# Performance work log

Measured on AMD Instinct MI355X. Metric: run time of the kernel, lower is better.

Reference implementation:

```python
import jax, jax.numpy as jnp
import numpy as np

EPS = 1e-5

def _bn_relu(x, gamma, beta):
    # BatchNorm2d in training mode: biased batch stats over (B, H, W)
    mu = jnp.mean(x, axis=(0, 2, 3), keepdims=True)
    var = jnp.mean((x - mu) ** 2, axis=(0, 2, 3), keepdims=True)
    xh = (x - mu) * jax.lax.rsqrt(var + EPS)
    return jax.nn.relu(xh * gamma[None, :, None, None] + beta[None, :, None, None])

def setup_inputs() -> dict:
    key = jax.random.key(0)
    ks = jax.random.split(key, 16)
    B, N, D = 4, 256, 256            # in_channels = 2*D = 512
    feats = jax.random.normal(ks[0], (B, 1 + 2 * N, D), dtype=jnp.float32)
    def lin(k, o, c):
        return jax.random.normal(k, (o, c), dtype=jnp.float32) * (1.0 / np.sqrt(c))
    return {
        "feats": feats,
        "W1": lin(ks[1], 256, 512), "b1": jnp.zeros((256,), jnp.float32),
        "g1": jnp.ones((256,), jnp.float32), "be1": jnp.zeros((256,), jnp.float32),
        "W2": lin(ks[2], 128, 256), "b2": jnp.zeros((128,), jnp.float32),
        "g2": jnp.ones((128,), jnp.float32), "be2": jnp.zeros((128,), jnp.float32),
        "W3": lin(ks[3], 64, 128), "b3": jnp.zeros((64,), jnp.float32),
        "g3": jnp.ones((64,), jnp.float32), "be3": jnp.zeros((64,), jnp.float32),
        "W4": lin(ks[4], 1, 64), "b4": jnp.zeros((1,), jnp.float32),
    }

def reference(feats, W1, b1, g1, be1, W2, b2, g2, be2, W3, b3, g3, be3, W4, b4):
    B, T, Dfull = feats.shape
    f = feats[:, 1:]                                  # [B, 2N, D]
    N = f.shape[1] // 2
    D = f.shape[2]
    f = f.reshape(B, N, 2, D).mean(axis=2)            # [B, N, D]
    fc = jnp.transpose(f, (0, 2, 1))                  # [B, D, N]
    # conv1(cat(x, t)) fused: first D input channels see f_i, last D see f_j
    a = jnp.einsum('oc,bcn->bon', W1[:, :D], fc)      # [B, 256, N]
    bpart = jnp.einsum('oc,bcn->bon', W1[:, D:], fc)  # [B, 256, N]
    h = a[:, :, :, None] + bpart[:, :, None, :] + b1[None, :, None, None]  # [B,256,N,N]
    h = _bn_relu(h, g1, be1)
    h = jnp.einsum('oc,bcij->boij', W2, h) + b2[None, :, None, None]
    h = _bn_relu(h, g2, be2)
    h = jnp.einsum('oc,bcij->boij', W3, h) + b3[None, :, None, None]
    h = _bn_relu(h, g3, be3)
    h = jnp.einsum('oc,bcij->boij', W4, h) + b4[None, :, None, None]
    return h[:, 0]                                    # [B, N, N]
```

## Files before the change

### kernel.cpp

```cpp
#include <hip/hip_runtime.h>
#include <hip/hip_bf16.h>

#define EPS 1e-5f

typedef __attribute__((ext_vector_type(8))) short bf16x8;
typedef __attribute__((ext_vector_type(4))) float f32x4;

static constexpr size_t OFF_FT    = 0;
static constexpr size_t OFF_W1T   = 1048576;
static constexpr size_t OFF_W2B   = 1572864;
static constexpr size_t OFF_W3B   = 1638400;
static constexpr size_t OFF_S1    = 1654784;
static constexpr size_t OFF_T1    = 1655808;
static constexpr size_t OFF_ST2   = 1660928;
static constexpr size_t OFF_ABT   = 1703936;
static constexpr size_t OFF_H2T   = 4194304;
static constexpr size_t OFF_P1    = OFF_H2T;
static constexpr size_t OFF_H3T   = 71303168;

static __device__ inline float bfu2f(unsigned int u16) {
    return __uint_as_float(u16 << 16);
}
static __device__ inline unsigned short f2bfu(float f) {
    unsigned int u = __float_as_uint(f);
    unsigned int r = u + 0x7fffu + ((u >> 16) & 1u);
    return (unsigned short)(r >> 16);
}
static __device__ inline unsigned int pkbf(float lo, float hi) {
    __hip_bfloat162 p = __float22bfloat162_rn(make_float2(lo, hi));
    return *reinterpret_cast<unsigned int*>(&p);
}

static __device__ __forceinline__ uint2 bnpk4(float4 fv, const float* aa, const float* ss, int c) {
    float4 a4 = *(const float4*)(aa + c);
    float4 s4 = *(const float4*)(ss + c);
    float r0 = fmaxf(fmaf(fv.x, s4.x, a4.x), 0.f);
    float r1 = fmaxf(fmaf(fv.y, s4.y, a4.y), 0.f);
    float r2 = fmaxf(fmaf(fv.z, s4.z, a4.z), 0.f);
    float r3 = fmaxf(fmaf(fv.w, s4.w, a4.w), 0.f);
    return make_uint2(pkbf(r0, r1), pkbf(r2, r3));
}
static __device__ __forceinline__ uint2 bn2pk4(uint2 v, const float* ss, const float* tt, int c) {
    float4 s4 = *(const float4*)(ss + c);
    float4 t4 = *(const float4*)(tt + c);
    float r0 = fmaxf(fmaf(bfu2f(v.x & 0xffffu), s4.x, t4.x), 0.f);
    float r1 = fmaxf(fmaf(bfu2f(v.x >> 16),     s4.y, t4.y), 0.f);
    float r2 = fmaxf(fmaf(bfu2f(v.y & 0xffffu), s4.z, t4.z), 0.f);
    float r3 = fmaxf(fmaf(bfu2f(v.y >> 16),     s4.w, t4.w), 0.f);
    return make_uint2(pkbf(r0, r1), pkbf(r2, r3));
}

__global__ __launch_bounds__(256) void k0kt(const float* __restrict__ feats,
                                            const float* __restrict__ W1,
                                            const float* __restrict__ W2,
                                            const float* __restrict__ W3,
                                            float* __restrict__ fT, float* __restrict__ W1T,
                                            unsigned short* __restrict__ W2b,
                                            unsigned short* __restrict__ W3b,
                                            float* __restrict__ statsZero) {
    int bx = blockIdx.x, tid = threadIdx.x;
    if (bx < 128) {
        __shared__ float s[32][65];
        int b = bx >> 5, nt = (bx >> 2) & 7, ct = bx & 3;
        int n0 = nt * 32, c0 = ct * 64;
        const float* fb = feats + (size_t)b * 513 * 256;
        #pragma unroll
        for (int k = 0; k < 8; ++k) {
            int idx = tid + k * 256;
            int n = idx >> 6, c = idx & 63;
            const float* r = fb + (size_t)(1 + 2 * (n0 + n)) * 256 + c0 + c;
            s[n][c] = 0.5f * (r[0] + r[256]);
        }
        __syncthreads();
        #pragma unroll
        for (int k = 0; k < 8; ++k) {
            int idx = tid + k * 256;
            int c = idx >> 5, n = idx & 31;
            fT[((size_t)(b * 256) + c0 + c) * 256 + n0 + n] = s[n][c];
        }
    } else {
        if (bx == 128) {
            #pragma unroll
            for (int z = 0; z < 13; ++z) {
                int f = tid + z * 256;
                if (f < 3073) statsZero[f] = 0.f;
            }
        }
        int idx = (bx - 128) * 256 + tid;
        if (idx < 131072) {
            int c = idx >> 9, o = idx & 511;
            W1T[idx] = (o < 256) ? W1[(size_t)o * 512 + c] : W1[(size_t)(o - 256) * 512 + 256 + c];
        } else if (idx < 163840) {
            int j = idx - 131072;
            W2b[j] = f2bfu(W2[j]);
        } else if (idx < 172032) {
            int j = idx - 163840;
            W3b[j] = f2bfu(W3[j]);
        }
    }
}

__global__ __launch_bounds__(256) void k1_gemm(const float* __restrict__ W1T,
                                               const float* __restrict__ fT,
                                               float* __restrict__ abT,
                                               float2* __restrict__ part,
                                               const float* __restrict__ g1,
                                               const float* __restrict__ be1,
                                               float* __restrict__ s1,
                                               float* __restrict__ t1,
                                               unsigned int* __restrict__ counter) {
    __shared__ float sW[64][36];
    __shared__ float sF[64][68];
    int tid = threadIdx.x;
    int bx = blockIdx.x;
    int b = bx >> 2, n0 = (bx & 3) * 64;
    int o0 = blockIdx.y * 32;
    int og = tid >> 4, jq = tid & 15;
    float acc[2][4] = {};
    for (int c0 = 0; c0 < 256; c0 += 64) {
        #pragma unroll
        for (int k = 0; k < 8; ++k) {
            int idx = tid + k * 256;
            int c = idx >> 5, o = idx & 31;
            sW[c][o] = W1T[(size_t)(c0 + c) * 512 + o0 + o];
        }
        #pragma unroll
        for (int k = 0; k < 16; ++k) {
            int idx = tid + k * 256;
            int c = idx >> 6, n = idx & 63;
            sF[c][n] = fT[((size_t)(b * 256) + c0 + c) * 256 + n0 + n];
        }
        __syncthreads();
        #pragma unroll 8
        for (int c = 0; c < 64; ++c) {
            float4 rv = *(const float4*)&sF[c][jq * 4];
            float2 wv = *(const float2*)&sW[c][og * 2];
            float rr[4] = {rv.x, rv.y, rv.z, rv.w};
            #pragma unroll
            for (int w = 0; w < 4; ++w) {
                acc[0][w] = fmaf(wv.x, rr[w], acc[0][w]);
                acc[1][w] = fmaf(wv.y, rr[w], acc[1][w]);
            }
        }
        __syncthreads();
    }
    #pragma unroll
    for (int w = 0; w < 4; ++w) {
        int n = n0 + jq * 4 + w;
        *(float2*)&abT[((size_t)(b * 256) + n) * 512 + o0 + og * 2] =
            make_float2(acc[0][w], acc[1][w]);
    }
    #pragma unroll
    for (int m = 0; m < 2; ++m) {
        float s = 0.f, q = 0.f;
        #pragma unroll
        for (int w = 0; w < 4; ++w) { float v = acc[m][w]; s += v; q += v * v; }
        #pragma unroll
        for (int off = 8; off; off >>= 1) { s += __shfl_down(s, off); q += __shfl_down(q, off); }
        if (jq == 0) part[(size_t)bx * 512 + o0 + og * 2 + m] = make_float2(s, q);
    }
    __threadfence();
    __shared__ unsigned int lastFlag;
    if (tid == 0) lastFlag = (atomicAdd(counter, 1u) == 255u) ? 1u : 0u;
    __syncthreads();
    if (lastFlag) {
        int o = tid;
        float msum = 0.f, e2sum = 0.f;
        #pragma unroll
        for (int bb = 0; bb < 4; ++bb) {
            float Sa = 0.f, Qa = 0.f, Sb = 0.f, Qb = 0.f;
            #pragma unroll
            for (int nt = 0; nt < 4; ++nt) {
                float2 pa = part[(size_t)(bb * 4 + nt) * 512 + o];
                float2 pb = part[(size_t)(bb * 4 + nt) * 512 + 256 + o];
                Sa += pa.x; Qa += pa.y; Sb += pb.x; Qb += pb.y;
            }
            float ma = Sa * (1.f / 256.f), mb = Sb * (1.f / 256.f);
            msum += ma + mb;
            e2sum += Qa * (1.f / 256.f) + Qb * (1.f / 256.f) + 2.f * ma * mb;
        }
        float m = msum * 0.25f, e2 = e2sum * 0.25f;
        float var = e2 - m * m;
        float s = g1[o] * rsqrtf(var + EPS);
        s1[o] = s;
        t1[o] = be1[o] - m * s;
    }
}

__global__ __launch_bounds__(256) void k2_mfma(const float* __restrict__ abT,
                                               const unsigned short* __restrict__ W2b,
                                               const float* __restrict__ s1,
                                               const float* __restrict__ t1,
                                               unsigned short* __restrict__ h2T,
                                               float* __restrict__ gS2,
                                               float* __restrict__ gQ2) {
    __shared__ __align__(16) char smem[35840];
    float* aaS = (float*)smem;
    float* ssS = (float*)(smem + 1024);
    unsigned short* sW = (unsigned short*)(smem + 2048);
    unsigned short* sB = (unsigned short*)(smem + 12288);
    unsigned short* sT = (unsigned short*)smem;
    float* sS = (float*)(smem + 34816);
    float* sQ = (float*)(smem + 35328);

    int tid = threadIdx.x;
    int j0 = blockIdx.x * 128, i = blockIdx.y, b = blockIdx.z;

    {
        float av = abT[((size_t)(b * 256 + i)) * 512 + tid];
        float s = s1[tid];
        aaS[tid] = fmaf(av, s, t1[tid]);
        ssS[tid] = s;
    }
    if (tid < 128) { sS[tid] = 0.f; sQ[tid] = 0.f; }
    __syncthreads();

    int lane = tid & 63, wv = tid >> 6;
    int wr = wv >> 1, wc = wv & 1;
    int lo = lane & 15, khi = lane >> 4;
    int jrow = tid >> 1, half = tid & 1;

    const float* bpRow = abT + ((size_t)(b * 256 + j0 + jrow)) * 512 + 256 + half * 16;
    const unsigned short* wRow = W2b + jrow * 256 + half * 16;

    f32x4 acc[4][4] = {};

    for (int c0 = 0; c0 < 256; c0 += 32) {
        {
            uint4 v0 = *(const uint4*)(wRow + c0);
            uint4 v1 = *(const uint4*)(wRow + c0 + 8);
            uint4* dst = (uint4*)(sW + jrow * 40 + half * 16);
            dst[0] = v0; dst[1] = v1;
        }
        {
            float4 f0 = *(const float4*)(bpRow + c0);
            float4 f1 = *(const float4*)(bpRow + c0 + 4);
            float4 f2 = *(const float4*)(bpRow + c0 + 8);
            float4 f3 = *(const float4*)(bpRow + c0 + 12);
            int cb = c0 + half * 16;
            uint2 p0 = bnpk4(f0, aaS, ssS, cb);
            uint2 p1 = bnpk4(f1, aaS, ssS, cb + 4);
            uint2 p2 = bnpk4(f2, aaS, ssS, cb + 8);
            uint2 p3 = bnpk4(f3, aaS, ssS, cb + 12);
            uint4* dst = (uint4*)(sB + jrow * 40 + half * 16);
            dst[0] = make_uint4(p0.x, p0.y, p1.x, p1.y);
            dst[1] = make_uint4(p2.x, p2.y, p3.x, p3.y);
        }
        __syncthreads();
        const unsigned short* aB = sW + (wr * 64 + lo) * 40 + khi * 8;
        const unsigned short* bB = sB + (wc * 64 + lo) * 40 + khi * 8;
        bf16x8 af[4], bfr[4];
        #pragma unroll
        for (int fm = 0; fm < 4; ++fm) af[fm] = *(const bf16x8*)(aB + fm * 16 * 40);
        #pragma unroll
        for (int fn = 0; fn < 4; ++fn) bfr[fn] = *(const bf16x8*)(bB + fn * 16 * 40);
        #pragma unroll
        for (int fm = 0; fm < 4; ++fm)
            #pragma unroll
            for (int fn = 0; fn < 4; ++fn)
                acc[fm][fn] = __builtin_amdgcn_mfma_f32_16x16x32_bf16(af[fm], bfr[fn], acc[fm][fn], 0, 0, 0);
        __syncthreads();
    }

    #pragma unroll
    for (int fm = 0; fm < 4; ++fm)
        #pragma unroll
        for (int fn = 0; fn < 4; ++fn) {
            int oq = wr * 64 + fm * 16 + khi * 4;
            int j  = wc * 64 + fn * 16 + lo;
            *(uint2*)(sT + j * 136 + oq) =
                make_uint2(pkbf(acc[fm][fn][0], acc[fm][fn][1]),
                           pkbf(acc[fm][fn][2], acc[fm][fn][3]));
        }
    __syncthreads();
    {
        size_t gbase = (((size_t)(b * 256 + i)) * 256 + j0 + jrow) * 128 + half * 64;
        #pragma unroll
        for (int e = 0; e < 8; ++e) {
            uint4 v = *(const uint4*)(sT + jrow * 136 + half * 64 + e * 8);
            *(uint4*)(h2T + gbase + e * 8) = v;
        }
    }
    {
        int o = tid & 127, p = tid >> 7;
        const unsigned short* col = sT + (p * 64) * 136 + o;
        float s = 0.f, q = 0.f;
        for (int j = 0; j < 64; ++j) {
            float v = bfu2f(col[j * 136]);
            s += v; q += v * v;
        }
        atomicAdd(&sS[o], s);
        atomicAdd(&sQ[o], q);
    }
    __syncthreads();
    if (tid < 128) {
        int slot = (i & 7) * 128;
        atomicAdd(&gS2[slot + tid], sS[tid]);
        atomicAdd(&gQ2[slot + tid], sQ[tid]);
    }
}

__global__ __launch_bounds__(256) void k3_mfma(const unsigned short* __restrict__ h2T,
                                               const unsigned short* __restrict__ W3b,
                                               const float* __restrict__ gS2,
                                               const float* __restrict__ gQ2,
                                               const float* __restrict__ g2,
                                               const float* __restrict__ be2,
                                               unsigned short* __restrict__ h3T,
                                               float* __restrict__ gS3,
                                               float* __restrict__ gQ3) {
    __shared__ __align__(16) char smem[39424];
    float* s2S = (float*)smem;
    float* t2S = (float*)(smem + 512);
    unsigned short* sW3 = (unsigned short*)(smem + 1024);
    unsigned short* sB  = (unsigned short*)(smem + 18432);
    float* sS = (float*)(smem + 38912);
    float* sQ = (float*)(smem + 39168);
    unsigned short* sT  = (unsigned short*)(smem + 1024);

    int tid = threadIdx.x;
    int i = blockIdx.x, b = blockIdx.y;
    if (tid < 128) {
        float su = 0.f, qu = 0.f;
        #pragma unroll
        for (int k = 0; k < 8; ++k) { su += gS2[k * 128 + tid]; qu += gQ2[k * 128 + tid]; }
        float mean = su * (1.f / 262144.f);
        float var = qu * (1.f / 262144.f) - mean * mean;
        float sc = g2[tid] * rsqrtf(var + EPS);
        s2S[tid] = sc;
        t2S[tid] = be2[tid] - mean * sc;
    }
    if (tid < 64) { sS[tid] = 0.f; sQ[tid] = 0.f; }
    {
        int o = tid >> 2, qd = tid & 3;
        #pragma unroll
        for (int e = 0; e < 4; ++e) {
            uint4 v = *(const uint4*)(W3b + o * 128 + qd * 32 + e * 8);
            *(uint4*)(sW3 + o * 136 + qd * 32 + e * 8) = v;
        }
    }
    __syncthreads();

    int lane = tid & 63, wv = tid >> 6;
    int lo = lane & 15, khi = lane >> 4;

    f32x4 acc[4][4] = {};
    const unsigned short* src = h2T + (((size_t)(b * 256 + i)) * 256 + tid) * 128;

    for (int c0 = 0; c0 < 128; c0 += 32) {
        #pragma unroll
        for (int e = 0; e < 4; ++e) {
            uint4 v = *(const uint4*)(src + c0 + e * 8);
            int c = c0 + e * 8;
            uint2 pa = bn2pk4(make_uint2(v.x, v.y), s2S, t2S, c);
            uint2 pb = bn2pk4(make_uint2(v.z, v.w), s2S, t2S, c + 4);
            *(uint4*)(sB + tid * 40 + e * 8) = make_uint4(pa.x, pa.y, pb.x, pb.y);
        }
        __syncthreads();
        bf16x8 af[4], bfr[4];
        #pragma unroll
        for (int fm = 0; fm < 4; ++fm)
            af[fm] = *(const bf16x8*)(sW3 + (fm * 16 + lo) * 136 + c0 + khi * 8);
        #pragma unroll
        for (int fn = 0; fn < 4; ++fn)
            bfr[fn] = *(const bf16x8*)(sB + (wv * 64 + fn * 16 + lo) * 40 + khi * 8);
        #pragma unroll
        for (int fm = 0; fm < 4; ++fm)
            #pragma unroll
            for (int fn = 0; fn < 4; ++fn)
                acc[fm][fn] = __builtin_amdgcn_mfma_f32_16x16x32_bf16(af[fm], bfr[fn], acc[fm][fn], 0, 0, 0);
        __syncthreads();
    }

    #pragma unroll
    for (int fm = 0; fm < 4; ++fm)
        #pragma unroll
        for (int fn = 0; fn < 4; ++fn) {
            int oq = fm * 16 + khi * 4;
            int j  = wv * 64 + fn * 16 + lo;
            *(uint2*)(sT + j * 72 + oq) =
                make_uint2(pkbf(acc[fm][fn][0], acc[fm][fn][1]),
                           pkbf(acc[fm][fn][2], acc[fm][fn][3]));
        }
    __syncthreads();
    {
        size_t gbase = (((size_t)(b * 256 + i)) * 256 + tid) * 64;
        #pragma unroll
        for (int e = 0; e < 8; ++e) {
            uint4 v = *(const uint4*)(sT + tid * 72 + e * 8);
            *(uint4*)(h3T + gbase + e * 8) = v;
        }
    }
    {
        int o = tid & 63, p = tid >> 6;
        const unsigned short* col = sT + (p * 64) * 72 + o;
        float s = 0.f, q = 0.f;
        for (int j = 0; j < 64; ++j) {
            float v = bfu2f(col[j * 72]);
            s += v; q += v * v;
        }
        atomicAdd(&sS[o], s);
        atomicAdd(&sQ[o], q);
    }
    __syncthreads();
    if (tid < 64) {
        int slot = (i & 7) * 64;
        atomicAdd(&gS3[slot + tid], sS[tid]);
        atomicAdd(&gQ3[slot + tid], sQ[tid]);
    }
}

__global__ __launch_bounds__(256) void k4_final(const unsigned short* __restrict__ h3T,
                                                const float* __restrict__ W4,
                                                const float* __restrict__ gS3,
                                                const float* __restrict__ gQ3,
                                                const float* __restrict__ g3,
                                                const float* __restrict__ be3,
                                                const float* __restrict__ b4,
                                                float* __restrict__ out) {
    __shared__ __align__(16) char smem[37632];
    float* wS = (float*)smem;
    float* sS = (float*)(smem + 256);
    float* tS = (float*)(smem + 512);
    unsigned short* sL = (unsigned short*)(smem + 768);
    int tid = threadIdx.x;
    int i = blockIdx.x, b = blockIdx.y;
    if (tid < 64) {
        float su = 0.f, qu = 0.f;
        #pragma unroll
        for (int k = 0; k < 8; ++k) { su += gS3[k * 64 + tid]; qu += gQ3[k * 64 + tid]; }
        float mean = su * (1.f / 262144.f);
        float var = qu * (1.f / 262144.f) - mean * mean;
        float sc = g3[tid] * rsqrtf(var + EPS);
        wS[tid] = W4[tid];
        sS[tid] = sc;
        tS[tid] = be3[tid] - mean * sc;
    }
    const unsigned short* src = h3T + ((size_t)(b * 256 + i)) * 256 * 64;
    #pragma unroll
    for (int e = 0; e < 8; ++e) {
        int f = tid + 256 * e;
        uint4 v = *(const uint4*)(src + f * 8);
        *(uint4*)(sL + (f >> 3) * 72 + (f & 7) * 8) = v;
    }
    __syncthreads();
    float acc = 0.f;
    #pragma unroll
    for (int e = 0; e < 8; ++e) {
        uint4 v = *(const uint4*)(sL + tid * 72 + e * 8);
        unsigned int w[4] = {v.x, v.y, v.z, v.w};
        #pragma unroll
        for (int k = 0; k < 4; ++k) {
            int c = e * 8 + 2 * k;
            float f0 = bfu2f(w[k] & 0xffffu);
            float f1 = bfu2f(w[k] >> 16);
            acc += wS[c] * fmaxf(fmaf(f0, sS[c], tS[c]), 0.f);
            acc += wS[c + 1] * fmaxf(fmaf(f1, sS[c + 1], tS[c + 1]), 0.f);
        }
    }
    out[((size_t)(b * 256 + i)) * 256 + tid] = acc + b4[0];
}

extern "C" void kernel_launch(void* const* d_in, const int* in_sizes, int n_in,
                              void* d_out, int out_size, void* d_ws, size_t ws_size,
                              hipStream_t stream) {
    const float* feats = (const float*)d_in[0];
    const float* W1  = (const float*)d_in[1];
    const float* g1  = (const float*)d_in[3];
    const float* be1 = (const float*)d_in[4];
    const float* W2  = (const float*)d_in[5];
    const float* g2  = (const float*)d_in[7];
    const float* be2 = (const float*)d_in[8];
    const float* W3  = (const float*)d_in[9];
    const float* g3  = (const float*)d_in[11];
    const float* be3 = (const float*)d_in[12];
    const float* W4  = (const float*)d_in[13];
    const float* b4  = (const float*)d_in[14];

    char* ws = (char*)d_ws;
    float* fT   = (float*)(ws + OFF_FT);
    float* W1T  = (float*)(ws + OFF_W1T);
    unsigned short* W2b = (unsigned short*)(ws + OFF_W2B);
    unsigned short* W3b = (unsigned short*)(ws + OFF_W3B);
    float* abT  = (float*)(ws + OFF_ABT);
    float* s1   = (float*)(ws + OFF_S1);
    float* t1   = (float*)(ws + OFF_T1);
    float* gS2  = (float*)(ws + OFF_ST2);
    float* gQ2  = (float*)(ws + OFF_ST2 + 4096);
    float* gS3  = (float*)(ws + OFF_ST2 + 8192);
    float* gQ3  = (float*)(ws + OFF_ST2 + 10240);
    unsigned int* counter = (unsigned int*)(ws + OFF_ST2 + 12288);
    float2* part = (float2*)(ws + OFF_P1);
    unsigned short* h2T = (unsigned short*)(ws + OFF_H2T);
    unsigned short* h3T = (unsigned short*)(ws + OFF_H3T);
    float* out = (float*)d_out;

    k0kt<<<800, 256, 0, stream>>>(feats, W1, W2, W3, fT, W1T, W2b, W3b, (float*)(ws + OFF_ST2));
    k1_gemm<<<dim3(16, 16), 256, 0, stream>>>(W1T, fT, abT, part, g1, be1, s1, t1, counter);
    k2_mfma<<<dim3(2, 256, 4), 256, 0, stream>>>(abT, W2b, s1, t1, h2T, gS2, gQ2);
    k3_mfma<<<dim3(256, 4), 256, 0, stream>>>(h2T, W3b, gS2, gQ2, g2, be2, h3T, gS3, gQ3);
    k4_final<<<dim3(256, 4), 256, 0, stream>>>(h3T, W4, gS3, gQ3, g3, be3, b4, out);
}
```

Before: 220.5 us.

## Widen k2 tile to cover all 256 j columns per block

The second-layer MFMA kernel now has each block compute the full 256-wide j range for one (i,b) row instead of two 128-wide halves. The point is to load each W2 tile into shared memory once per row instead of twice and to halve the block count. The epilogue stages results through shared memory in two 64-channel passes to fit the larger tile. The cost is 8x4 accumulators per thread, which raises register pressure and may lower occupancy, and only 1024 blocks remain.

Measured after the change: 283.6 us. 28.6% more time.

```diff
diff --git a/kernel.cpp b/kernel.cpp
--- a/kernel.cpp
+++ b/kernel.cpp
@@ -194,17 +194,17 @@
                                                unsigned short* __restrict__ h2T,
                                                float* __restrict__ gS2,
                                                float* __restrict__ gQ2) {
-    __shared__ __align__(16) char smem[35840];
+    __shared__ __align__(16) char smem[39936];
     float* aaS = (float*)smem;
     float* ssS = (float*)(smem + 1024);
-    unsigned short* sW = (unsigned short*)(smem + 2048);
-    unsigned short* sB = (unsigned short*)(smem + 12288);
-    unsigned short* sT = (unsigned short*)smem;
-    float* sS = (float*)(smem + 34816);
-    float* sQ = (float*)(smem + 35328);
+    float* sS  = (float*)(smem + 2048);
+    float* sQ  = (float*)(smem + 2560);
+    unsigned short* sW = (unsigned short*)(smem + 3072);
+    unsigned short* sB = (unsigned short*)(smem + 13312);
+    unsigned short* sT = (unsigned short*)(smem + 3072);
 
     int tid = threadIdx.x;
-    int j0 = blockIdx.x * 128, i = blockIdx.y, b = blockIdx.z;
+    int i = blockIdx.x, b = blockIdx.y;
 
     {
         float av = abT[((size_t)(b * 256 + i)) * 512 + tid];
@@ -218,18 +218,17 @@
     int lane = tid & 63, wv = tid >> 6;
     int wr = wv >> 1, wc = wv & 1;
     int lo = lane & 15, khi = lane >> 4;
-    int jrow = tid >> 1, half = tid & 1;
-
-    const float* bpRow = abT + ((size_t)(b * 256 + j0 + jrow)) * 512 + 256 + half * 16;
-    const unsigned short* wRow = W2b + jrow * 256 + half * 16;
-
-    f32x4 acc[4][4] = {};
+
+    const float* bpRow = abT + ((size_t)(b * 256 + tid)) * 512 + 256;
+    const unsigned short* wRow = W2b + (tid >> 1) * 256 + (tid & 1) * 16;
+
+    f32x4 acc[4][8] = {};
 
     for (int c0 = 0; c0 < 256; c0 += 32) {
         {
             uint4 v0 = *(const uint4*)(wRow + c0);
             uint4 v1 = *(const uint4*)(wRow + c0 + 8);
-            uint4* dst = (uint4*)(sW + jrow * 40 + half * 16);
+            uint4* dst = (uint4*)(sW + (tid >> 1) * 40 + (tid & 1) * 16);
             dst[0] = v0; dst[1] = v1;
         }
         {
@@ -237,60 +236,75 @@
             float4 f1 = *(const float4*)(bpRow + c0 + 4);
             float4 f2 = *(const float4*)(bpRow + c0 + 8);
             float4 f3 = *(const float4*)(bpRow + c0 + 12);
-            int cb = c0 + half * 16;
-            uint2 p0 = bnpk4(f0, aaS, ssS, cb);
-            uint2 p1 = bnpk4(f1, aaS, ssS, cb + 4);
-            uint2 p2 = bnpk4(f2, aaS, ssS, cb + 8);
-            uint2 p3 = bnpk4(f3, aaS, ssS, cb + 12);
-            uint4* dst = (uint4*)(sB + jrow * 40 + half * 16);
+            float4 f4 = *(const float4*)(bpRow + c0 + 16);
+            float4 f5 = *(const float4*)(bpRow + c0 + 20);
+            float4 f6 = *(const float4*)(bpRow + c0 + 24);
+            float4 f7 = *(const float4*)(bpRow + c0 + 28);
+            uint2 p0 = bnpk4(f0, aaS, ssS, c0);
+            uint2 p1 = bnpk4(f1, aaS, ssS, c0 + 4);
+            uint2 p2 = bnpk4(f2, aaS, ssS, c0 + 8);
+            uint2 p3 = bnpk4(f3, aaS, ssS, c0 + 12);
+            uint2 p4 = bnpk4(f4, aaS, ssS, c0 + 16);
+            uint2 p5 = bnpk4(f5, aaS, ssS, c0 + 20);
+            uint2 p6 = bnpk4(f6, aaS, ssS, c0 + 24);
+            uint2 p7 = bnpk4(f7, aaS, ssS, c0 + 28);
+            uint4* dst = (uint4*)(sB + tid * 40);
             dst[0] = make_uint4(p0.x, p0.y, p1.x, p1.y);
             dst[1] = make_uint4(p2.x, p2.y, p3.x, p3.y);
+            dst[2] = make_uint4(p4.x, p4.y, p5.x, p5.y);
+            dst[3] = make_uint4(p6.x, p6.y, p7.x, p7.y);
         }
         __syncthreads();
         const unsigned short* aB = sW + (wr * 64 + lo) * 40 + khi * 8;
-        const unsigned short* bB = sB + (wc * 64 + lo) * 40 + khi * 8;
-        bf16x8 af[4], bfr[4];
+        const unsigned short* bB = sB + (wc * 128 + lo) * 40 + khi * 8;
+        bf16x8 af[4], bfr[8];
         #pragma unroll
         for (int fm = 0; fm < 4; ++fm) af[fm] = *(const bf16x8*)(aB + fm * 16 * 40);
         #pragma unroll
-        for (int fn = 0; fn < 4; ++fn) bfr[fn] = *(const bf16x8*)(bB + fn * 16 * 40);
+        for (int fn = 0; fn < 8; ++fn) bfr[fn] = *(const bf16x8*)(bB + fn * 16 * 40);
         #pragma unroll
         for (int fm = 0; fm < 4; ++fm)
             #pragma unroll
-            for (int fn = 0; fn < 4; ++fn)
+            for (int fn = 0; fn < 8; ++fn)
                 acc[fm][fn] = __builtin_amdgcn_mfma_f32_16x16x32_bf16(af[fm], bfr[fn], acc[fm][fn], 0, 0, 0);
         __syncthreads();
     }
 
     #pragma unroll
-    for (int fm = 0; fm < 4; ++fm)
-        #pragma unroll
-        for (int fn = 0; fn < 4; ++fn) {
-            int oq = wr * 64 + fm * 16 + khi * 4;
-            int j  = wc * 64 + fn * 16 + lo;
-            *(uint2*)(sT + j * 136 + oq) =
-                make_uint2(pkbf(acc[fm][fn][0], acc[fm][fn][1]),
-                           pkbf(acc[fm][fn][2], acc[fm][fn][3]));
-        }
-    __syncthreads();
-    {
-        size_t gbase = (((size_t)(b * 256 + i)) * 256 + j0 + jrow) * 128 + half * 64;
-        #pragma unroll
-        for (int e = 0; e < 8; ++e) {
-            uint4 v = *(const uint4*)(sT + jrow * 136 + half * 64 + e * 8);
-            *(uint4*)(h2T + gbase + e * 8) = v;
-        }
-    }
-    {
-        int o = tid & 127, p = tid >> 7;
-        const unsigned short* col = sT + (p * 64) * 136 + o;
-        float s = 0.f, q = 0.f;
-        for (int j = 0; j < 64; ++j) {
-            float v = bfu2f(col[j * 136]);
-            s += v; q += v * v;
-        }
-        atomicAdd(&sS[o], s);
-        atomicAdd(&sQ[o], q);
+    for (int rr = 0; rr < 2; ++rr) {
+        __syncthreads();
+        if (wr == rr) {
+            #pragma unroll
+            for (int fm = 0; fm < 4; ++fm)
+                #pragma unroll
+                for (int fn = 0; fn < 8; ++fn) {
+                    int oq = fm * 16 + khi * 4;
+                    int j  = wc * 128 + fn * 16 + lo;
+                    *(uint2*)(sT + j * 72 + oq) =
+                        make_uint2(pkbf(acc[fm][fn][0], acc[fm][fn][1]),
+                                   pkbf(acc[fm][fn][2], acc[fm][fn][3]));
+                }
+        }
+        __syncthreads();
+        {
+            size_t gbase = (((size_t)(b * 256 + i)) * 256 + tid) * 128 + rr * 64;
+            #pragma unroll
+            for (int e = 0; e < 8; ++e) {
+                uint4 v = *(const uint4*)(sT + tid * 72 + e * 8);
+                *(uint4*)(h2T + gbase + e * 8) = v;
+            }
+        }
+        {
+            int o = tid & 63, p = tid >> 6;
+            const unsigned short* col = sT + (p * 64) * 72 + o;
+            float s = 0.f, q = 0.f;
+            for (int j = 0; j < 64; ++j) {
+                float v = bfu2f(col[j * 72]);
+                s += v; q += v * v;
+            }
+            atomicAdd(&sS[rr * 64 + o], s);
+            atomicAdd(&sQ[rr * 64 + o], q);
+        }
     }
     __syncthreads();
     if (tid < 128) {
@@ -497,7 +511,7 @@
 
     k0kt<<<800, 256, 0, stream>>>(feats, W1, W2, W3, fT, W1T, W2b, W3b, (float*)(ws + OFF_ST2));
     k1_gemm<<<dim3(16, 16), 256, 0, stream>>>(W1T, fT, abT, part, g1, be1, s1, t1, counter);
-    k2_mfma<<<dim3(2, 256, 4), 256, 0, stream>>>(abT, W2b, s1, t1, h2T, gS2, gQ2);
+    k2_mfma<<<dim3(256, 4), 256, 0, stream>>>(abT, W2b, s1, t1, h2T, gS2, gQ2);
     k3_mfma<<<dim3(256, 4), 256, 0, stream>>>(h2T, W3b, gS2, gQ2, g2, be2, h3T, gS3, gQ3);
     k4_final<<<dim3(256, 4), 256, 0, stream>>>(h3T, W4, gS3, gQ3, g3, be3, b4, out);
 }
```
